# Performance work log

Hardware: AMD Instinct MI355X
Metric: run time of the kernel (lower is better)

The kernel has to match this reference:

```python
import jax, jax.numpy as jnp
import numpy as np

B, S, H, F, E, K = 2, 2048, 1024, 4096, 8, 2


def setup_inputs() -> dict:
    key = jax.random.key(0)
    ks = jax.random.split(key, 5)
    scale = 0.02
    return {
        "hidden_states": jax.random.normal(ks[0], (B, S, H), jnp.float32),
        "gate_w": jax.random.normal(ks[1], (H, E), jnp.float32) * scale,  # nn.Linear(H,E,bias=False)
        "w1": jax.random.normal(ks[2], (E, H, F), jnp.float32) * scale,   # per-expert fc1
        "b1": jnp.zeros((E, F), jnp.float32),
        "w2": jax.random.normal(ks[3], (E, F, H), jnp.float32) * scale,   # per-expert fc2
        "b2": jnp.zeros((E, H), jnp.float32),
    }


def reference(hidden_states, gate_w, w1, b1, w2, b2):
    b, s, h = hidden_states.shape
    x = hidden_states.reshape(b * s, h)  # [T, H]
    T = x.shape[0]
    n_experts = gate_w.shape[1]

    # --- Top-K gating ---
    router_logits = x @ gate_w                      # [T, E]
    router_probs = jax.nn.softmax(router_logits, axis=-1)
    topk_probs, topk_idx = jax.lax.top_k(router_probs, K)  # [T, K]
    topk_probs = topk_probs / topk_probs.sum(axis=-1, keepdims=True)
    aux_loss = n_experts * jnp.sum(router_probs.mean(axis=0) ** 2)

    # --- Combine weights: scatter normalized top-k probs into dense [T, E] ---
    combine_w = jnp.zeros((T, n_experts), x.dtype).at[
        jnp.arange(T)[:, None], topk_idx
    ].add(topk_probs)

    # --- Expert MLPs (dense per-expert batched GEMM; zero combine weight drops unrouted) ---
    hidden = jax.nn.relu(jnp.einsum('th,ehf->etf', x, w1) + b1[:, None, :])  # [E, T, F]
    expert_out = jnp.einsum('etf,efh->eth', hidden, w2) + b2[:, None, :]     # [E, T, H]

    out = jnp.einsum('te,eth->th', combine_w, expert_out)  # weighted combine
    return out.reshape(b, s, h), aux_loss
```

## Files before the change

### kernel.cpp

```cpp
#include <hip/hip_runtime.h>
#include <hip/hip_bf16.h>
#include <cstdint>

#define AS1 __attribute__((address_space(1)))
#define AS3 __attribute__((address_space(3)))

typedef __attribute__((ext_vector_type(8))) short short8x;
typedef __attribute__((ext_vector_type(4))) float f32x4;

static constexpr int T    = 4096;
static constexpr int HD   = 1024;
static constexpr int FD   = 4096;
static constexpr int NE   = 8;
static constexpr int P    = T * 2;
static constexpr int PPAD = P + 128;
static constexpr int MAXTILES = P / 128 + NE;
static constexpr int RTB  = 16;
static constexpr int RNB  = T / RTB;

struct TileDesc { int e; int start; int rows; int pad; };

__device__ __forceinline__ uint16_t f2bf(float f) {
  uint32_t u = __builtin_bit_cast(uint32_t, f);
  u += 0x7FFFu + ((u >> 16) & 1u);
  return (uint16_t)(u >> 16);
}
__device__ __forceinline__ float bf2f(uint16_t b) {
  uint32_t u = ((uint32_t)b) << 16;
  return __builtin_bit_cast(float, u);
}

__device__ __forceinline__ void gload_lds16(const void* g, void* l) {
  __builtin_amdgcn_global_load_lds((const AS1 uint32_t*)g, (AS3 uint32_t*)l, 16, 0, 0);
}

__global__ __launch_bounds__(256) void cvt_x_kernel(const float* __restrict__ x,
                                                    uint16_t* __restrict__ xb) {
  size_t i = ((size_t)blockIdx.x * 256 + threadIdx.x) * 4;
  float4 v = *(const float4*)&x[i];
  ushort4 o;
  o.x = f2bf(v.x); o.y = f2bf(v.y); o.z = f2bf(v.z); o.w = f2bf(v.w);
  *(ushort4*)&xb[i] = o;
}

__global__ __launch_bounds__(256) void transpose_cvt_kernel(
    const float* __restrict__ in, uint16_t* __restrict__ out, int R, int C) {
  __shared__ float tile[32][33];
  int z = blockIdx.z;
  const float* inp = in + (size_t)z * R * C;
  uint16_t* outp = out + (size_t)z * R * C;
  int tx = threadIdx.x, ty = threadIdx.y;
  int r0 = blockIdx.y * 32, c0 = blockIdx.x * 32;
#pragma unroll
  for (int j = 0; j < 4; ++j)
    tile[ty + 8 * j][tx] = inp[(size_t)(r0 + ty + 8 * j) * C + (c0 + tx)];
  __syncthreads();
#pragma unroll
  for (int j = 0; j < 4; ++j)
    outp[(size_t)(c0 + ty + 8 * j) * R + (r0 + tx)] = f2bf(tile[tx][ty + 8 * j]);
}

__global__ __launch_bounds__(256) void router_kernel(
    const float* __restrict__ x, const float* __restrict__ gate_w,
    int* __restrict__ topk_idx, float* __restrict__ topk_w,
    float* __restrict__ part_sums, int* __restrict__ part_counts) {
  __shared__ float g[NE * HD];
  __shared__ float ls[NE];
  __shared__ int   lc[NE];
  int tid = threadIdx.x;
  for (int i = tid; i < NE * HD; i += 256)
    g[(i & 7) * HD + (i >> 3)] = gate_w[i];
  if (tid < NE) { ls[tid] = 0.f; lc[tid] = 0; }
  __syncthreads();
  int wave = tid >> 6, lane = tid & 63;
  float psum[NE];
#pragma unroll
  for (int e = 0; e < NE; ++e) psum[e] = 0.f;

  for (int tt = 0; tt < RTB / 4; ++tt) {
    int t = blockIdx.x * RTB + wave * (RTB / 4) + tt;
    const float* xr = x + (size_t)t * HD;
    float acc[NE];
#pragma unroll
    for (int e = 0; e < NE; ++e) acc[e] = 0.f;
    for (int i = 0; i < HD / 64; ++i) {
      float xv = xr[lane + i * 64];
#pragma unroll
      for (int e = 0; e < NE; ++e) acc[e] += xv * g[e * HD + lane + i * 64];
    }
#pragma unroll
    for (int off = 32; off > 0; off >>= 1)
#pragma unroll
      for (int e = 0; e < NE; ++e) acc[e] += __shfl_down(acc[e], off);
    if (lane == 0) {
      float m = acc[0];
#pragma unroll
      for (int e = 1; e < NE; ++e) m = fmaxf(m, acc[e]);
      float p[NE], s = 0.f;
#pragma unroll
      for (int e = 0; e < NE; ++e) { p[e] = expf(acc[e] - m); s += p[e]; }
      float inv = 1.f / s;
#pragma unroll
      for (int e = 0; e < NE; ++e) { p[e] *= inv; psum[e] += p[e]; }
      int i0 = 0;
#pragma unroll
      for (int e = 1; e < NE; ++e) if (p[e] > p[i0]) i0 = e;
      int i1 = (i0 == 0) ? 1 : 0;
#pragma unroll
      for (int e = 0; e < NE; ++e) if (e != i0 && e != i1 && p[e] > p[i1]) i1 = e;
      float wsum = p[i0] + p[i1];
      topk_idx[t * 2] = i0; topk_idx[t * 2 + 1] = i1;
      topk_w[t * 2] = p[i0] / wsum; topk_w[t * 2 + 1] = p[i1] / wsum;
      atomicAdd(&lc[i0], 1); atomicAdd(&lc[i1], 1);
    }
  }
  if (lane == 0)
#pragma unroll
    for (int e = 0; e < NE; ++e) atomicAdd(&ls[e], psum[e]);
  __syncthreads();
  if (tid < NE) {
    part_sums[blockIdx.x * NE + tid]   = ls[tid];
    part_counts[blockIdx.x * NE + tid] = lc[tid];
  }
}

__global__ __launch_bounds__(64) void finalize_kernel(
    const int* __restrict__ part_counts, const float* __restrict__ part_sums,
    int* __restrict__ offsets, TileDesc* __restrict__ desc,
    int* __restrict__ ntiles, float* __restrict__ aux_out) {
  __shared__ int   csh[NE];
  __shared__ float ssh[NE];
  int tid = threadIdx.x;
  if (tid < NE) {
    int c = 0; float s = 0.f;
    for (int b = 0; b < RNB; ++b) {
      c += part_counts[b * NE + tid];
      s += part_sums[b * NE + tid];
    }
    csh[tid] = c; ssh[tid] = s;
  }
  __syncthreads();
  if (tid == 0) {
    int off = 0, nt = 0;
    for (int e = 0; e < NE; ++e) {
      offsets[e] = off;
      int c = csh[e];
      for (int i = 0; i < c; i += 128) {
        int rows = c - i; if (rows > 128) rows = 128;
        desc[nt].e = e; desc[nt].start = off + i; desc[nt].rows = rows; desc[nt].pad = 0;
        nt++;
      }
      off += c;
    }
    *ntiles = nt;
    float aux = 0.f;
    for (int e = 0; e < NE; ++e) {
      float mean = ssh[e] / (float)T;
      aux += mean * mean;
    }
    *aux_out = (float)NE * aux;
  }
}

__global__ __launch_bounds__(256) void scatter_kernel(
    const int* __restrict__ topk_idx, const int* __restrict__ offsets,
    int* __restrict__ fill, int* __restrict__ pair_tok, int* __restrict__ tok_pos) {
  int t = blockIdx.x * 256 + threadIdx.x;
  int lane = threadIdx.x & 63;
  unsigned long long below = (lane == 63) ? ~0ull >> 1
                                          : ((1ull << (lane + 1)) - 1) >> 1;
#pragma unroll
  for (int k = 0; k < 2; ++k) {
    int e = topk_idx[t * 2 + k];
    int pos = 0;
    for (int ex = 0; ex < NE; ++ex) {
      unsigned long long m = __ballot(e == ex);
      if (e == ex) {
        int leader = __ffsll((long long)m) - 1;
        int cnt = __popcll(m);
        int base = 0;
        if (lane == leader) base = atomicAdd(&fill[ex], cnt);
        base = __shfl(base, leader);
        pos = base + __popcll(m & below);
      }
    }
    int pp = offsets[e] + pos;
    pair_tok[pp] = t;
    tok_pos[t * 2 + k] = pp;
  }
}

template <int KD, int ND, int EPI>
__global__ __launch_bounds__(256) void moe_gemm(
    const uint16_t* __restrict__ Abase, const int* __restrict__ pair_tok,
    const uint16_t* __restrict__ Bw, const float* __restrict__ bias,
    uint16_t* __restrict__ Cout, const TileDesc* __restrict__ desc,
    const int* __restrict__ ntiles) {
  int mt = blockIdx.y;
  if (mt >= *ntiles) return;
  TileDesc d = desc[mt];
  int nb = blockIdx.x;

  __shared__ uint16_t As[128 * 32];
  __shared__ uint16_t Bs[128 * 32];
  __shared__ int rowA[128];

  int tid = threadIdx.x, lane = tid & 63, wave = tid >> 6;
  int wm = wave >> 1, wn = wave & 1;

  int idx0 = (wave * 2 + 0) * 64 + lane;
  int idx1 = (wave * 2 + 1) * 64 + lane;
  int ar0 = idx0 >> 2, kc0 = idx0 & 3;
  int ar1 = idx1 >> 2, kc1 = idx1 & 3;

  int ra0, ra1;
  if constexpr (EPI == 0) {
    if (tid < 128) rowA[tid] = (tid < d.rows) ? pair_tok[d.start + tid] : 0;
    __syncthreads();
    ra0 = rowA[ar0]; ra1 = rowA[ar1];
  } else {
    ra0 = d.start + ar0; ra1 = d.start + ar1;
  }

  const uint16_t* Bbase = Bw + ((size_t)d.e * ND + (size_t)nb * 128) * KD;

  f32x4 acc[4][4];
#pragma unroll
  for (int i = 0; i < 4; ++i)
#pragma unroll
    for (int j = 0; j < 4; ++j) acc[i][j] = (f32x4){0.f, 0.f, 0.f, 0.f};

  for (int kt = 0; kt < KD / 32; ++kt) {
    if (kt) __syncthreads();
    int kb = kt * 32;
    gload_lds16(Abase + (size_t)ra0 * KD + kb + kc0 * 8, &As[(wave * 2 + 0) * 512]);
    gload_lds16(Abase + (size_t)ra1 * KD + kb + kc1 * 8, &As[(wave * 2 + 1) * 512]);
    gload_lds16(Bbase + (size_t)ar0 * KD + kb + kc0 * 8, &Bs[(wave * 2 + 0) * 512]);
    gload_lds16(Bbase + (size_t)ar1 * KD + kb + kc1 * 8, &Bs[(wave * 2 + 1) * 512]);
    __syncthreads();

    short8x af[4], bfr[4];
#pragma unroll
    for (int i = 0; i < 4; ++i)
      af[i] = *(const short8x*)&As[(wm * 64 + i * 16 + (lane & 15)) * 32 + (lane >> 4) * 8];
#pragma unroll
    for (int j = 0; j < 4; ++j)
      bfr[j] = *(const short8x*)&Bs[(wn * 64 + j * 16 + (lane & 15)) * 32 + (lane >> 4) * 8];
#pragma unroll
    for (int i = 0; i < 4; ++i)
#pragma unroll
      for (int j = 0; j < 4; ++j)
        acc[i][j] = __builtin_amdgcn_mfma_f32_16x16x32_bf16(af[i], bfr[j], acc[i][j], 0, 0, 0);
  }

  int rq = (lane >> 4) * 4;
  int cl = lane & 15;
#pragma unroll
  for (int i = 0; i < 4; ++i) {
    int rb = wm * 64 + i * 16 + rq;
#pragma unroll
    for (int j = 0; j < 4; ++j) {
      int col = nb * 128 + wn * 64 + j * 16 + cl;
      float bv = bias[d.e * ND + col];
#pragma unroll
      for (int q = 0; q < 4; ++q) {
        int r = rb + q;
        if (r < d.rows) {
          float v = acc[i][j][q] + bv;
          if (EPI == 0) v = fmaxf(v, 0.f);
          Cout[(size_t)(d.start + r) * ND + col] = f2bf(v);
        }
      }
    }
  }
}

__global__ __launch_bounds__(256) void combine_kernel(
    const uint16_t* __restrict__ po, const int* __restrict__ tok_pos,
    const float* __restrict__ topk_w, float* __restrict__ out) {
  int t = blockIdx.x;
  int c = threadIdx.x * 4;
  int p0 = tok_pos[t * 2], p1 = tok_pos[t * 2 + 1];
  float w0 = topk_w[t * 2], w1 = topk_w[t * 2 + 1];
  ushort4 a = *(const ushort4*)&po[(size_t)p0 * HD + c];
  ushort4 b = *(const ushort4*)&po[(size_t)p1 * HD + c];
  float4 o;
  o.x = w0 * bf2f(a.x) + w1 * bf2f(b.x);
  o.y = w0 * bf2f(a.y) + w1 * bf2f(b.y);
  o.z = w0 * bf2f(a.z) + w1 * bf2f(b.z);
  o.w = w0 * bf2f(a.w) + w1 * bf2f(b.w);
  *(float4*)&out[(size_t)t * HD + c] = o;
}

extern "C" void kernel_launch(void* const* d_in, const int* in_sizes, int n_in,
                              void* d_out, int out_size, void* d_ws, size_t ws_size,
                              hipStream_t stream) {
  const float* x      = (const float*)d_in[0];
  const float* gate_w = (const float*)d_in[1];
  const float* w1     = (const float*)d_in[2];
  const float* b1     = (const float*)d_in[3];
  const float* w2     = (const float*)d_in[4];
  const float* b2     = (const float*)d_in[5];
  float* out = (float*)d_out;
  (void)in_sizes; (void)n_in; (void)out_size; (void)ws_size;

  char* w = (char*)d_ws;
  size_t off = 0;
  auto alloc = [&](size_t bytes) -> void* {
    void* p = w + off;
    off = (off + bytes + 255) & ~(size_t)255;
    return p;
  };
  int*      meta     = (int*)alloc(256);
  int*      fill     = meta;
  int*      offsets  = (int*)alloc(256);
  int*      ntiles   = offsets + 8;
  TileDesc* desc     = (TileDesc*)alloc(sizeof(TileDesc) * 128);
  int*      topk_idx = (int*)alloc(sizeof(int) * P);
  float*    topk_w   = (float*)alloc(sizeof(float) * P);
  int*      tok_pos  = (int*)alloc(sizeof(int) * P);
  int*      pair_tok = (int*)alloc(sizeof(int) * PPAD);
  float*    psums    = (float*)alloc(sizeof(float) * RNB * NE);
  int*      pcounts  = (int*)alloc(sizeof(int) * RNB * NE);
  uint16_t* xb       = (uint16_t*)alloc((size_t)T * HD * 2);
  uint16_t* w1t      = (uint16_t*)alloc((size_t)NE * FD * HD * 2);
  uint16_t* w2t      = (uint16_t*)alloc((size_t)NE * HD * FD * 2);
  uint16_t* hidden   = (uint16_t*)alloc((size_t)PPAD * FD * 2);
  uint16_t* pout     = (uint16_t*)alloc((size_t)PPAD * HD * 2);

  hipMemsetAsync(meta, 0, 256, stream);
  cvt_x_kernel<<<(T * HD) / 1024, 256, 0, stream>>>(x, xb);
  transpose_cvt_kernel<<<dim3(FD / 32, HD / 32, NE), dim3(32, 8), 0, stream>>>(w1, w1t, HD, FD);
  transpose_cvt_kernel<<<dim3(HD / 32, FD / 32, NE), dim3(32, 8), 0, stream>>>(w2, w2t, FD, HD);
  router_kernel<<<RNB, 256, 0, stream>>>(x, gate_w, topk_idx, topk_w, psums, pcounts);
  finalize_kernel<<<1, 64, 0, stream>>>(pcounts, psums, offsets, desc, ntiles,
                                        out + (size_t)T * HD);
  scatter_kernel<<<T / 256, 256, 0, stream>>>(topk_idx, offsets, fill, pair_tok, tok_pos);
  moe_gemm<HD, FD, 0><<<dim3(FD / 128, MAXTILES), 256, 0, stream>>>(
      xb, pair_tok, w1t, b1, hidden, desc, ntiles);
  moe_gemm<FD, HD, 1><<<dim3(HD / 128, MAXTILES), 256, 0, stream>>>(
      hidden, pair_tok, w2t, b2, pout, desc, ntiles);
  combine_kernel<<<T, 256, 0, stream>>>(pout, tok_pos, topk_w, out);
}
```

Measured before the change: 390.2 us.

## Add 256x256 double-buffered swizzled fc1 GEMM and vectorize weight transpose

```diff
diff --git a/kernel.cpp b/kernel.cpp
--- a/kernel.cpp
+++ b/kernel.cpp
@@ -4,6 +4,7 @@
 
 #define AS1 __attribute__((address_space(1)))
 #define AS3 __attribute__((address_space(3)))
+#define SBAR() asm volatile("s_barrier" ::: "memory")
 
 typedef __attribute__((ext_vector_type(8))) short short8x;
 typedef __attribute__((ext_vector_type(4))) float f32x4;
@@ -13,8 +14,9 @@
 static constexpr int FD   = 4096;
 static constexpr int NE   = 8;
 static constexpr int P    = T * 2;
-static constexpr int PPAD = P + 128;
-static constexpr int MAXTILES = P / 128 + NE;
+static constexpr int PPAD = P + 256;
+static constexpr int MAXTILES  = P / 128 + NE;
+static constexpr int MAXT256   = P / 256 + NE;
 static constexpr int RTB  = 16;
 static constexpr int RNB  = T / RTB;
 
@@ -45,19 +47,33 @@
 
 __global__ __launch_bounds__(256) void transpose_cvt_kernel(
     const float* __restrict__ in, uint16_t* __restrict__ out, int R, int C) {
-  __shared__ float tile[32][33];
+  __shared__ float tile[64][65];
   int z = blockIdx.z;
   const float* inp = in + (size_t)z * R * C;
   uint16_t* outp = out + (size_t)z * R * C;
-  int tx = threadIdx.x, ty = threadIdx.y;
-  int r0 = blockIdx.y * 32, c0 = blockIdx.x * 32;
-#pragma unroll
-  for (int j = 0; j < 4; ++j)
-    tile[ty + 8 * j][tx] = inp[(size_t)(r0 + ty + 8 * j) * C + (c0 + tx)];
+  int r0 = blockIdx.y * 64, c0 = blockIdx.x * 64;
+  int tid = threadIdx.x;
+  int lr = tid >> 4;
+  int lc4 = (tid & 15) * 4;
+#pragma unroll
+  for (int p = 0; p < 4; ++p) {
+    float4 v = *(const float4*)&inp[(size_t)(r0 + lr + p * 16) * C + c0 + lc4];
+    tile[lr + p * 16][lc4 + 0] = v.x;
+    tile[lr + p * 16][lc4 + 1] = v.y;
+    tile[lr + p * 16][lc4 + 2] = v.z;
+    tile[lr + p * 16][lc4 + 3] = v.w;
+  }
   __syncthreads();
 #pragma unroll
-  for (int j = 0; j < 4; ++j)
-    outp[(size_t)(c0 + ty + 8 * j) * R + (r0 + tx)] = f2bf(tile[tx][ty + 8 * j]);
+  for (int p = 0; p < 4; ++p) {
+    int c = lr + p * 16;
+    ushort4 o;
+    o.x = f2bf(tile[lc4 + 0][c]);
+    o.y = f2bf(tile[lc4 + 1][c]);
+    o.z = f2bf(tile[lc4 + 2][c]);
+    o.w = f2bf(tile[lc4 + 3][c]);
+    *(ushort4*)&outp[(size_t)(c0 + c) * R + r0 + lc4] = o;
+  }
 }
 
 __global__ __launch_bounds__(256) void router_kernel(
@@ -126,8 +142,8 @@
 
 __global__ __launch_bounds__(64) void finalize_kernel(
     const int* __restrict__ part_counts, const float* __restrict__ part_sums,
-    int* __restrict__ offsets, TileDesc* __restrict__ desc,
-    int* __restrict__ ntiles, float* __restrict__ aux_out) {
+    int* __restrict__ offsets, TileDesc* __restrict__ desc, TileDesc* __restrict__ desc256,
+    int* __restrict__ ntiles, int* __restrict__ ntiles256, float* __restrict__ aux_out) {
   __shared__ int   csh[NE];
   __shared__ float ssh[NE];
   int tid = threadIdx.x;
@@ -141,7 +157,7 @@
   }
   __syncthreads();
   if (tid == 0) {
-    int off = 0, nt = 0;
+    int off = 0, nt = 0, nt2 = 0;
     for (int e = 0; e < NE; ++e) {
       offsets[e] = off;
       int c = csh[e];
@@ -150,9 +166,15 @@
         desc[nt].e = e; desc[nt].start = off + i; desc[nt].rows = rows; desc[nt].pad = 0;
         nt++;
       }
+      for (int i = 0; i < c; i += 256) {
+        int rows = c - i; if (rows > 256) rows = 256;
+        desc256[nt2].e = e; desc256[nt2].start = off + i; desc256[nt2].rows = rows; desc256[nt2].pad = 0;
+        nt2++;
+      }
       off += c;
     }
     *ntiles = nt;
+    *ntiles256 = nt2;
     float aux = 0.f;
     for (int e = 0; e < NE; ++e) {
       float mean = ssh[e] / (float)T;
@@ -190,12 +212,182 @@
   }
 }
 
-template <int KD, int ND, int EPI>
-__global__ __launch_bounds__(256) void moe_gemm(
-    const uint16_t* __restrict__ Abase, const int* __restrict__ pair_tok,
-    const uint16_t* __restrict__ Bw, const float* __restrict__ bias,
-    uint16_t* __restrict__ Cout, const TileDesc* __restrict__ desc,
-    const int* __restrict__ ntiles) {
+__global__ __launch_bounds__(512, 2) void moe_fc1_256(
+    const uint16_t* __restrict__ xb, const int* __restrict__ pair_tok,
+    const uint16_t* __restrict__ w1t, const float* __restrict__ bias,
+    uint16_t* __restrict__ hidden, const TileDesc* __restrict__ desc256,
+    const int* __restrict__ ntiles256) {
+  constexpr int KD = HD;
+  constexpr int ND = FD;
+  constexpr int NBC = ND / 256;
+  constexpr int NT = KD / 64;
+  constexpr int GRID = NBC * MAXT256;
+
+  extern __shared__ char smem[];
+  uint16_t* lds = (uint16_t*)smem;
+  int* rowA = (int*)(smem + 131072);
+
+  int orig = blockIdx.x;
+  int work = (orig & 7) * (GRID / 8) + (orig >> 3);
+  int nb = work % NBC;
+  int mt = work / NBC;
+  if (mt >= *ntiles256) return;
+  TileDesc d = desc256[mt];
+
+  int tid = threadIdx.x, lane = tid & 63, wave = tid >> 6;
+  int wm = wave >> 2, wn = wave & 3;
+
+  if (tid < 256) rowA[tid] = (tid < d.rows) ? pair_tok[d.start + tid] : 0;
+  __syncthreads();
+
+  int wl8 = wave * 8 + (lane >> 3);
+  int colel = ((lane & 7) << 3) ^ (((lane >> 5) & 1) << 4);
+  const uint16_t* Asrc[2][2];
+  const uint16_t* Bsrc[2][2];
+#pragma unroll
+  for (int h = 0; h < 2; ++h)
+#pragma unroll
+    for (int i = 0; i < 2; ++i) {
+      int lr = h * 128 + i * 64 + wl8;
+      Asrc[h][i] = xb + (size_t)rowA[lr] * KD + colel;
+      Bsrc[h][i] = w1t + ((size_t)d.e * ND + nb * 256 + lr) * KD + colel;
+    }
+
+  auto stage = [&](int slot, int kt) {
+    int ko = kt * 64;
+#pragma unroll
+    for (int h = 0; h < 2; ++h)
+#pragma unroll
+      for (int i = 0; i < 2; ++i) {
+        int dst = slot * 16384 + h * 8192 + i * 4096 + wave * 512;
+        gload_lds16(Asrc[h][i] + ko, &lds[dst]);
+        gload_lds16(Bsrc[h][i] + ko, &lds[32768 + dst]);
+      }
+  };
+
+  int laneRd = (lane & 15) * 64 + (((lane >> 4) * 8) ^ (((lane >> 2) & 1) << 4));
+
+  f32x4 acc[8][4];
+#pragma unroll
+  for (int i = 0; i < 8; ++i)
+#pragma unroll
+    for (int j = 0; j < 4; ++j) acc[i][j] = (f32x4){0.f, 0.f, 0.f, 0.f};
+
+  short8x aq[4][2], b0[2][2], b1[2][2];
+
+  stage(0, 0);
+  stage(1, 1);
+  asm volatile("s_waitcnt vmcnt(8)" ::: "memory");
+  SBAR();
+
+  for (int kt = 0; kt < NT; ++kt) {
+    int slot = kt & 1;
+    int Ab = slot * 16384 + wm * 8192;
+    int Bb = 32768 + slot * 16384 + (wn >> 1) * 8192 + (wn & 1) * 4096;
+
+#pragma unroll
+    for (int fm = 0; fm < 4; ++fm)
+#pragma unroll
+      for (int ks = 0; ks < 2; ++ks)
+        aq[fm][ks] = *(const short8x*)&lds[Ab + fm * 1024 + ks * 32 + laneRd];
+#pragma unroll
+    for (int fn = 0; fn < 2; ++fn)
+#pragma unroll
+      for (int ks = 0; ks < 2; ++ks)
+        b0[fn][ks] = *(const short8x*)&lds[Bb + fn * 1024 + ks * 32 + laneRd];
+    SBAR();
+    __builtin_amdgcn_s_setprio(1);
+#pragma unroll
+    for (int fm = 0; fm < 4; ++fm)
+#pragma unroll
+      for (int fn = 0; fn < 2; ++fn)
+#pragma unroll
+        for (int ks = 0; ks < 2; ++ks)
+          acc[fm][fn] = __builtin_amdgcn_mfma_f32_16x16x32_bf16(aq[fm][ks], b0[fn][ks], acc[fm][fn], 0, 0, 0);
+    __builtin_amdgcn_s_setprio(0);
+    SBAR();
+
+#pragma unroll
+    for (int fn = 0; fn < 2; ++fn)
+#pragma unroll
+      for (int ks = 0; ks < 2; ++ks)
+        b1[fn][ks] = *(const short8x*)&lds[Bb + (fn + 2) * 1024 + ks * 32 + laneRd];
+    SBAR();
+    __builtin_amdgcn_s_setprio(1);
+#pragma unroll
+    for (int fm = 0; fm < 4; ++fm)
+#pragma unroll
+      for (int fn = 0; fn < 2; ++fn)
+#pragma unroll
+        for (int ks = 0; ks < 2; ++ks)
+          acc[fm][fn + 2] = __builtin_amdgcn_mfma_f32_16x16x32_bf16(aq[fm][ks], b1[fn][ks], acc[fm][fn + 2], 0, 0, 0);
+    __builtin_amdgcn_s_setprio(0);
+    SBAR();
+
+#pragma unroll
+    for (int fm = 0; fm < 4; ++fm)
+#pragma unroll
+      for (int ks = 0; ks < 2; ++ks)
+        aq[fm][ks] = *(const short8x*)&lds[Ab + 4096 + fm * 1024 + ks * 32 + laneRd];
+    SBAR();
+    __builtin_amdgcn_s_setprio(1);
+#pragma unroll
+    for (int fm = 0; fm < 4; ++fm)
+#pragma unroll
+      for (int fn = 0; fn < 2; ++fn)
+#pragma unroll
+        for (int ks = 0; ks < 2; ++ks)
+          acc[fm + 4][fn + 2] = __builtin_amdgcn_mfma_f32_16x16x32_bf16(aq[fm][ks], b1[fn][ks], acc[fm + 4][fn + 2], 0, 0, 0);
+    __builtin_amdgcn_s_setprio(0);
+    SBAR();
+
+    if (kt + 2 < NT) {
+      stage(slot, kt + 2);
+      asm volatile("s_waitcnt vmcnt(8)" ::: "memory");
+    } else {
+      asm volatile("s_waitcnt vmcnt(0)" ::: "memory");
+    }
+    __builtin_amdgcn_s_setprio(1);
+#pragma unroll
+    for (int fm = 0; fm < 4; ++fm)
+#pragma unroll
+      for (int fn = 0; fn < 2; ++fn)
+#pragma unroll
+        for (int ks = 0; ks < 2; ++ks)
+          acc[fm + 4][fn] = __builtin_amdgcn_mfma_f32_16x16x32_bf16(aq[fm][ks], b0[fn][ks], acc[fm + 4][fn], 0, 0, 0);
+    __builtin_amdgcn_s_setprio(0);
+    SBAR();
+  }
+
+  int rq = (lane >> 4) * 4, cl = lane & 15;
+  float bv[4];
+#pragma unroll
+  for (int fn = 0; fn < 4; ++fn)
+    bv[fn] = bias[d.e * ND + nb * 256 + wn * 64 + fn * 16 + cl];
+#pragma unroll
+  for (int fm = 0; fm < 8; ++fm) {
+    int rb = wm * 128 + fm * 16 + rq;
+#pragma unroll
+    for (int fn = 0; fn < 4; ++fn) {
+      int col = nb * 256 + wn * 64 + fn * 16 + cl;
+#pragma unroll
+      for (int q = 0; q < 4; ++q) {
+        int r = rb + q;
+        if (r < d.rows) {
+          float v = fmaxf(acc[fm][fn][q] + bv[fn], 0.f);
+          hidden[(size_t)(d.start + r) * ND + col] = f2bf(v);
+        }
+      }
+    }
+  }
+}
+
+__global__ __launch_bounds__(256) void moe_fc2_128(
+    const uint16_t* __restrict__ Abase, const uint16_t* __restrict__ Bw,
+    const float* __restrict__ bias, uint16_t* __restrict__ Cout,
+    const TileDesc* __restrict__ desc, const int* __restrict__ ntiles) {
+  constexpr int KD = FD;
+  constexpr int ND = HD;
   int mt = blockIdx.y;
   if (mt >= *ntiles) return;
   TileDesc d = desc[mt];
@@ -203,7 +395,6 @@
 
   __shared__ uint16_t As[128 * 32];
   __shared__ uint16_t Bs[128 * 32];
-  __shared__ int rowA[128];
 
   int tid = threadIdx.x, lane = tid & 63, wave = tid >> 6;
   int wm = wave >> 1, wn = wave & 1;
@@ -213,15 +404,7 @@
   int ar0 = idx0 >> 2, kc0 = idx0 & 3;
   int ar1 = idx1 >> 2, kc1 = idx1 & 3;
 
-  int ra0, ra1;
-  if constexpr (EPI == 0) {
-    if (tid < 128) rowA[tid] = (tid < d.rows) ? pair_tok[d.start + tid] : 0;
-    __syncthreads();
-    ra0 = rowA[ar0]; ra1 = rowA[ar1];
-  } else {
-    ra0 = d.start + ar0; ra1 = d.start + ar1;
-  }
-
+  int ra0 = d.start + ar0, ra1 = d.start + ar1;
   const uint16_t* Bbase = Bw + ((size_t)d.e * ND + (size_t)nb * 128) * KD;
 
   f32x4 acc[4][4];
@@ -261,13 +444,12 @@
 #pragma unroll
     for (int j = 0; j < 4; ++j) {
       int col = nb * 128 + wn * 64 + j * 16 + cl;
-      float bv = bias[d.e * ND + col];
+      float bvv = bias[d.e * ND + col];
 #pragma unroll
       for (int q = 0; q < 4; ++q) {
         int r = rb + q;
         if (r < d.rows) {
-          float v = acc[i][j][q] + bv;
-          if (EPI == 0) v = fmaxf(v, 0.f);
+          float v = acc[i][j][q] + bvv;
           Cout[(size_t)(d.start + r) * ND + col] = f2bf(v);
         }
       }
@@ -315,7 +497,9 @@
   int*      fill     = meta;
   int*      offsets  = (int*)alloc(256);
   int*      ntiles   = offsets + 8;
+  int*      ntiles256 = offsets + 9;
   TileDesc* desc     = (TileDesc*)alloc(sizeof(TileDesc) * 128);
+  TileDesc* desc256  = (TileDesc*)alloc(sizeof(TileDesc) * 64);
   int*      topk_idx = (int*)alloc(sizeof(int) * P);
   float*    topk_w   = (float*)alloc(sizeof(float) * P);
   int*      tok_pos  = (int*)alloc(sizeof(int) * P);
@@ -330,15 +514,15 @@
 
   hipMemsetAsync(meta, 0, 256, stream);
   cvt_x_kernel<<<(T * HD) / 1024, 256, 0, stream>>>(x, xb);
-  transpose_cvt_kernel<<<dim3(FD / 32, HD / 32, NE), dim3(32, 8), 0, stream>>>(w1, w1t, HD, FD);
-  transpose_cvt_kernel<<<dim3(HD / 32, FD / 32, NE), dim3(32, 8), 0, stream>>>(w2, w2t, FD, HD);
+  transpose_cvt_kernel<<<dim3(FD / 64, HD / 64, NE), 256, 0, stream>>>(w1, w1t, HD, FD);
+  transpose_cvt_kernel<<<dim3(HD / 64, FD / 64, NE), 256, 0, stream>>>(w2, w2t, FD, HD);
   router_kernel<<<RNB, 256, 0, stream>>>(x, gate_w, topk_idx, topk_w, psums, pcounts);
-  finalize_kernel<<<1, 64, 0, stream>>>(pcounts, psums, offsets, desc, ntiles,
-                                        out + (size_t)T * HD);
+  finalize_kernel<<<1, 64, 0, stream>>>(pcounts, psums, offsets, desc, desc256,
+                                        ntiles, ntiles256, out + (size_t)T * HD);
   scatter_kernel<<<T / 256, 256, 0, stream>>>(topk_idx, offsets, fill, pair_tok, tok_pos);
-  moe_gemm<HD, FD, 0><<<dim3(FD / 128, MAXTILES), 256, 0, stream>>>(
-      xb, pair_tok, w1t, b1, hidden, desc, ntiles);
-  moe_gemm<FD, HD, 1><<<dim3(HD / 128, MAXTILES), 256, 0, stream>>>(
-      hidden, pair_tok, w2t, b2, pout, desc, ntiles);
+  moe_fc1_256<<<(FD / 256) * MAXT256, 512, 131072 + 1024, stream>>>(
+      xb, pair_tok, w1t, b1, hidden, desc256, ntiles256);
+  moe_fc2_128<<<dim3(HD / 128, MAXTILES), 256, 0, stream>>>(
+      hidden, w2t, b2, pout, desc, ntiles);
   combine_kernel<<<T, 256, 0, stream>>>(pout, tok_pos, topk_w, out);
 }
```

Result: slower. 424.4 us (+8.7%).

## Remap MoE GEMM blocks per XCD and widen weight transpose tiles

Applied to the files above, without the earlier changes.

```diff
diff --git a/kernel.cpp b/kernel.cpp
--- a/kernel.cpp
+++ b/kernel.cpp
@@ -14,7 +14,7 @@
 static constexpr int NE   = 8;
 static constexpr int P    = T * 2;
 static constexpr int PPAD = P + 128;
-static constexpr int MAXTILES = P / 128 + NE;
+static constexpr int MAXT = P / 128 + NE;
 static constexpr int RTB  = 16;
 static constexpr int RNB  = T / RTB;
 
@@ -29,7 +29,6 @@
   uint32_t u = ((uint32_t)b) << 16;
   return __builtin_bit_cast(float, u);
 }
-
 __device__ __forceinline__ void gload_lds16(const void* g, void* l) {
   __builtin_amdgcn_global_load_lds((const AS1 uint32_t*)g, (AS3 uint32_t*)l, 16, 0, 0);
 }
@@ -45,19 +44,33 @@
 
 __global__ __launch_bounds__(256) void transpose_cvt_kernel(
     const float* __restrict__ in, uint16_t* __restrict__ out, int R, int C) {
-  __shared__ float tile[32][33];
+  __shared__ float tile[64][65];
   int z = blockIdx.z;
   const float* inp = in + (size_t)z * R * C;
   uint16_t* outp = out + (size_t)z * R * C;
-  int tx = threadIdx.x, ty = threadIdx.y;
-  int r0 = blockIdx.y * 32, c0 = blockIdx.x * 32;
-#pragma unroll
-  for (int j = 0; j < 4; ++j)
-    tile[ty + 8 * j][tx] = inp[(size_t)(r0 + ty + 8 * j) * C + (c0 + tx)];
+  int r0 = blockIdx.y * 64, c0 = blockIdx.x * 64;
+  int tid = threadIdx.x;
+  int lr = tid >> 4;
+  int lc4 = (tid & 15) * 4;
+#pragma unroll
+  for (int p = 0; p < 4; ++p) {
+    float4 v = *(const float4*)&inp[(size_t)(r0 + lr + p * 16) * C + c0 + lc4];
+    tile[lr + p * 16][lc4 + 0] = v.x;
+    tile[lr + p * 16][lc4 + 1] = v.y;
+    tile[lr + p * 16][lc4 + 2] = v.z;
+    tile[lr + p * 16][lc4 + 3] = v.w;
+  }
   __syncthreads();
 #pragma unroll
-  for (int j = 0; j < 4; ++j)
-    outp[(size_t)(c0 + ty + 8 * j) * R + (r0 + tx)] = f2bf(tile[tx][ty + 8 * j]);
+  for (int p = 0; p < 4; ++p) {
+    int c = lr + p * 16;
+    ushort4 o;
+    o.x = f2bf(tile[lc4 + 0][c]);
+    o.y = f2bf(tile[lc4 + 1][c]);
+    o.z = f2bf(tile[lc4 + 2][c]);
+    o.w = f2bf(tile[lc4 + 3][c]);
+    *(ushort4*)&outp[(size_t)(c0 + c) * R + r0 + lc4] = o;
+  }
 }
 
 __global__ __launch_bounds__(256) void router_kernel(
@@ -190,16 +203,23 @@
   }
 }
 
-template <int KD, int ND, int EPI>
+template <int KD, int ND, int NBG, int EPI>
 __global__ __launch_bounds__(256) void moe_gemm(
     const uint16_t* __restrict__ Abase, const int* __restrict__ pair_tok,
     const uint16_t* __restrict__ Bw, const float* __restrict__ bias,
     uint16_t* __restrict__ Cout, const TileDesc* __restrict__ desc,
     const int* __restrict__ ntiles) {
-  int mt = blockIdx.y;
+  constexpr int NB = ND / 128;
+  constexpr int SM = MAXT / 8;
+
+  int orig = blockIdx.x;
+  int xcd = orig & 7, local = orig >> 3;
+  int nbq = local / (SM * NBG);
+  int rem = local % (SM * NBG);
+  int mt  = xcd * SM + rem / NBG;
+  int nb  = nbq * NBG + rem % NBG;
   if (mt >= *ntiles) return;
   TileDesc d = desc[mt];
-  int nb = blockIdx.x;
 
   __shared__ uint16_t As[128 * 32];
   __shared__ uint16_t Bs[128 * 32];
@@ -330,15 +350,15 @@
 
   hipMemsetAsync(meta, 0, 256, stream);
   cvt_x_kernel<<<(T * HD) / 1024, 256, 0, stream>>>(x, xb);
-  transpose_cvt_kernel<<<dim3(FD / 32, HD / 32, NE), dim3(32, 8), 0, stream>>>(w1, w1t, HD, FD);
-  transpose_cvt_kernel<<<dim3(HD / 32, FD / 32, NE), dim3(32, 8), 0, stream>>>(w2, w2t, FD, HD);
+  transpose_cvt_kernel<<<dim3(FD / 64, HD / 64, NE), 256, 0, stream>>>(w1, w1t, HD, FD);
+  transpose_cvt_kernel<<<dim3(HD / 64, FD / 64, NE), 256, 0, stream>>>(w2, w2t, FD, HD);
   router_kernel<<<RNB, 256, 0, stream>>>(x, gate_w, topk_idx, topk_w, psums, pcounts);
   finalize_kernel<<<1, 64, 0, stream>>>(pcounts, psums, offsets, desc, ntiles,
                                         out + (size_t)T * HD);
   scatter_kernel<<<T / 256, 256, 0, stream>>>(topk_idx, offsets, fill, pair_tok, tok_pos);
-  moe_gemm<HD, FD, 0><<<dim3(FD / 128, MAXTILES), 256, 0, stream>>>(
+  moe_gemm<HD, FD, 4, 0><<<(FD / 128) * MAXT, 256, 0, stream>>>(
       xb, pair_tok, w1t, b1, hidden, desc, ntiles);
-  moe_gemm<FD, HD, 1><<<dim3(HD / 128, MAXTILES), 256, 0, stream>>>(
+  moe_gemm<FD, HD, 8, 1><<<(HD / 128) * MAXT, 256, 0, stream>>>(
       hidden, pair_tok, w2t, b2, pout, desc, ntiles);
   combine_kernel<<<T, 256, 0, stream>>>(pout, tok_pos, topk_w, out);
 }
```

Result: faster. 370.5 us (-5.1%).
